# Kernel tuning notes

Measured on AMD Instinct MI355X. Metric: run time of the kernel, lower is better.

The kernel has to match this reference:

```python
import jax, jax.numpy as jnp
import numpy as np

B, C, H, W, A = 16, 4, 256, 256, 6
EPS = 1e-5


def _bn(z, s, b):
    # train-mode BatchNorm with batch size 1: reduce over (H, W) per channel, biased var
    m = z.mean((1, 2), keepdims=True)
    v = ((z - m) ** 2).mean((1, 2), keepdims=True)
    return (z - m) * jax.lax.rsqrt(v + EPS) * s[:, None, None] + b[:, None, None]


def _conv(z, w, pad, dil=1):
    # z: [C_in, H, W], w: [C_out, C_in, kh, kw]
    return jax.lax.conv_general_dilated(
        z[None], w, (1, 1), [(pad, pad), (pad, pad)],
        rhs_dilation=(dil, dil), dimension_numbers=("NCHW", "OIHW", "NCHW"))[0]


def _up2_axis(z, axis):
    # bilinear x2 with align_corners=True along one axis
    n = z.shape[axis]
    m = 2 * n
    pos = jnp.arange(m, dtype=jnp.float32) * ((n - 1) / (m - 1))
    i0 = jnp.floor(pos).astype(jnp.int32)
    i1 = jnp.minimum(i0 + 1, n - 1)
    f = pos - i0
    shape = [1] * z.ndim
    shape[axis] = m
    f = f.reshape(shape).astype(z.dtype)
    return jnp.take(z, i0, axis=axis) * (1 - f) + jnp.take(z, i1, axis=axis) * f


def _up2(z):
    return _up2_axis(_up2_axis(z, 1), 2)


def setup_inputs():
    key = jax.random.key(0)
    ks = jax.random.split(key, 16)
    inp = {}
    inp["x"] = jax.random.normal(ks[0], (B, C, H, W), jnp.float32)
    inp["action"] = jax.random.randint(ks[1], (B,), 0, A)
    # (out_features, init variance 2/(out_ch*k*k)) matching the torch init
    specs = [(16 * C * 25, 2.0 / (16 * 25)), (16 * 16 * 25, 2.0 / (16 * 25)),
             (32 * 16 * 25, 2.0 / (32 * 25)), (32 * 32 * 25, 2.0 / (32 * 25)),
             (64 * 32 * 25, 2.0 / (64 * 25)), (64 * 64 * 25, 2.0 / (64 * 25)),
             (4 * 64, 2.0 / 4.0)]
    for i, (od, var) in enumerate(specs):
        inp[f"w{i + 1}"] = jax.random.normal(ks[2 + i], (od, A), jnp.float32) * float(np.sqrt(var))
        inp[f"b{i + 1}"] = jnp.zeros((od,), jnp.float32)
    for i, ch in enumerate([C, 16, 16, 32, 32, 64, 64]):
        inp[f"bn{i}_s"] = jnp.ones((ch,), jnp.float32)
        inp[f"bn{i}_b"] = jnp.zeros((ch,), jnp.float32)
    return inp


def reference(x, action, w1, b1, w2, b2, w3, b3, w4, b4, w5, b5, w6, b6, w7, b7,
              bn0_s, bn0_b, bn1_s, bn1_b, bn2_s, bn2_b, bn3_s, bn3_b,
              bn4_s, bn4_b, bn5_s, bn5_b, bn6_s, bn6_b):
    onehot = jax.nn.one_hot(action, A, dtype=x.dtype)  # [B, A]

    def gen(w, b, shape):
        return (onehot @ w.T + b).reshape((x.shape[0],) + shape)

    y1 = gen(w1, b1, (16, C, 5, 5))
    y2 = gen(w2, b2, (16, 16, 5, 5))
    y3 = gen(w3, b3, (32, 16, 5, 5))
    y4 = gen(w4, b4, (32, 32, 5, 5))
    y5 = gen(w5, b5, (64, 32, 5, 5))
    y6 = gen(w6, b6, (64, 64, 5, 5))
    y7 = gen(w7, b7, (4, 64, 1, 1))

    def single(xi, k1, k2, k3, k4, k5, k6, k7):
        r = jax.nn.relu(_bn(_conv(_bn(xi, bn0_s, bn0_b), k1, 4, 2), bn1_s, bn1_b))
        r = _bn(_conv(r, k2, 2), bn2_s, bn2_b)
        c, h, w_ = r.shape  # avg_pool2d k=2 s=2
        r = r.reshape(c, h // 2, 2, w_ // 2, 2).mean((2, 4))
        r = jax.nn.relu(_bn(_conv(r, k3, 4, 2), bn3_s, bn3_b))
        r = _bn(_conv(r, k4, 2), bn4_s, bn4_b)
        r = jax.nn.relu(_bn(_conv(r, k5, 4, 2), bn5_s, bn5_b))
        r = _bn(_conv(r, k6, 2), bn6_s, bn6_b)
        r = _conv(r, k7, 0)  # 1x1 conv to `classes` channels
        return _up2(r)

    out = jax.vmap(single)(x, y1, y2, y3, y4, y5, y6, y7)
    return out + x
```

## Files before the change

### kernel.cpp

```cpp
#include <hip/hip_runtime.h>

#define NB 16
#define NA 6

typedef __attribute__((ext_vector_type(8))) short short8;
typedef __attribute__((ext_vector_type(4))) short short4_;
typedef __attribute__((ext_vector_type(4))) float f32x4;
typedef __attribute__((ext_vector_type(4))) unsigned uint4_;
typedef __attribute__((ext_vector_type(2))) unsigned uint2_;

__device__ __forceinline__ short tobf(float f) {
    unsigned u = __builtin_bit_cast(unsigned, f);
    u += 0x7FFF + ((u >> 16) & 1);
    return (short)(u >> 16);
}
__device__ __forceinline__ float frombf(short s) {
    unsigned u = ((unsigned)(unsigned short)s) << 16;
    return __builtin_bit_cast(float, u);
}
__device__ __forceinline__ unsigned cvtpk(float a, float b) {
    unsigned r;
    asm("v_cvt_pk_bf16_f32 %0, %1, %2" : "=v"(r) : "v"(a), "v"(b));
    return r;
}

template<int CIN, int COUT>
__device__ __forceinline__ void pack_one(const float* __restrict__ w, const float* __restrict__ bias,
                                         int a, int b, short* __restrict__ dst, int j) {
    constexpr int KTOT = 25 * CIN;
    constexpr int KPAD = (KTOT + 31) & ~31;
    if (j >= COUT * KPAD) return;
    int oc = j / KPAD, k = j - oc * KPAD;
    float v = 0.f;
    if (k < KTOT) {
        int pos = k / CIN, ci = k - pos * CIN;
        int ky = pos / 5, kx = pos - ky * 5;
        int od = ((oc * CIN + ci) * 5 + ky) * 5 + kx;
        v = w[(size_t)od * NA + a] + bias[od];
    }
    dst[((size_t)(b * (KPAD / 8) + (k >> 3)) * COUT + oc) * 8 + (k & 7)] = tobf(v);
}

__global__ void pack_all(const float* __restrict__ w2, const float* __restrict__ b2,
                         const float* __restrict__ w3, const float* __restrict__ b3,
                         const float* __restrict__ w4, const float* __restrict__ b4,
                         const float* __restrict__ w5, const float* __restrict__ b5,
                         const float* __restrict__ w6, const float* __restrict__ b6,
                         const float* __restrict__ w1, const float* __restrict__ b1,
                         const float* __restrict__ w7, const float* __restrict__ b7,
                         const int* __restrict__ action,
                         short* __restrict__ d2, short* __restrict__ d3, short* __restrict__ d4,
                         short* __restrict__ d5, short* __restrict__ d6,
                         float* __restrict__ g1, float* __restrict__ g7) {
    const int b = blockIdx.y;
    const int a = action[b];
    const int bx = blockIdx.x;
    const int t = threadIdx.x;
    if (bx < 26)       pack_one<16, 16>(w2, b2, a, b, d2, bx * 256 + t);
    else if (bx < 78)  pack_one<16, 32>(w3, b3, a, b, d3, (bx - 26) * 256 + t);
    else if (bx < 178) pack_one<32, 32>(w4, b4, a, b, d4, (bx - 78) * 256 + t);
    else if (bx < 378) pack_one<32, 64>(w5, b5, a, b, d5, (bx - 178) * 256 + t);
    else if (bx < 778) pack_one<64, 64>(w6, b6, a, b, d6, (bx - 378) * 256 + t);
    else if (bx < 785) { int i = (bx - 778) * 256 + t;
                         if (i < 1600) g1[(size_t)b * 1600 + i] = w1[(size_t)i * NA + a] + b1[i]; }
    else               { g7[(size_t)b * 256 + t] = w7[(size_t)t * NA + a] + b7[t]; }
}

__global__ void stats0(const float* __restrict__ x, float* __restrict__ part0) {
    const int bc = blockIdx.y;
    const int b = bc >> 2, c = bc & 3;
    const float* p = x + ((size_t)bc << 16);
    const int base = blockIdx.x * 4096;
    float sum = 0.f, sq = 0.f;
    for (int i = threadIdx.x * 4; i < 4096; i += 1024) {
        float4 v = *(const float4*)(p + base + i);
        sum += (v.x + v.y) + (v.z + v.w);
        sq  += (v.x * v.x + v.y * v.y) + (v.z * v.z + v.w * v.w);
    }
#pragma unroll
    for (int off = 32; off > 0; off >>= 1) {
        sum += __shfl_down(sum, off);
        sq  += __shfl_down(sq, off);
    }
    __shared__ float ssum[4], ssq[4];
    int wv = threadIdx.x >> 6;
    if ((threadIdx.x & 63) == 0) { ssum[wv] = sum; ssq[wv] = sq; }
    __syncthreads();
    if (threadIdx.x == 0) {
        float S = ssum[0] + ssum[1] + ssum[2] + ssum[3];
        float Q = ssq[0] + ssq[1] + ssq[2] + ssq[3];
        atomicAdd(&part0[((size_t)b * 2 + 0) * 4 + c], S);
        atomicAdd(&part0[((size_t)b * 2 + 1) * 4 + c], Q);
    }
}

__global__ void bn0_apply(const float* __restrict__ x, short* __restrict__ a0,
                          const float* __restrict__ part0,
                          const float* __restrict__ sc0, const float* __restrict__ bi0) {
    int t = blockIdx.x * 256 + threadIdx.x;
    int b = t >> 16, px = t & 65535;
    f32x4 g, e;
#pragma unroll
    for (int c = 0; c < 4; ++c) {
        float S0 = part0[((size_t)b * 2 + 0) * 4 + c];
        float Q0 = part0[((size_t)b * 2 + 1) * 4 + c];
        float m = S0 * (1.f / 65536.f);
        float var = Q0 * (1.f / 65536.f) - m * m;
        float gg = sc0[c] * rsqrtf(var + 1e-5f);
        g[c] = gg;
        e[c] = bi0[c] - m * gg;
    }
    f32x4 f;
#pragma unroll
    for (int c = 0; c < 4; ++c)
        f[c] = x[(((size_t)b * 4 + c) << 16) + px] * g[c] + e[c];
    uint2_ o = {cvtpk(f[0], f[1]), cvtpk(f[2], f[3])};
    *(uint2_*)&a0[((size_t)t) * 4] = o;
}

__global__ void __launch_bounds__(256) conv1k(const short* __restrict__ a0,
                                              const float* __restrict__ w1g,
                                              short* __restrict__ c1,
                                              float* __restrict__ partout) {
    __shared__ float wf[1600];
    __shared__ short4_ tile[16 * 72];
    const int b = blockIdx.z;
    const int y0 = blockIdx.y * 8;
    const int x0 = blockIdx.x * 64;
    const int tid = threadIdx.x;
    for (int t = tid; t < 1600; t += 256) {
        int pos = t >> 6, ci = (t >> 4) & 3, oc = t & 15;
        wf[t] = w1g[b * 1600 + (oc * 4 + ci) * 25 + pos];
    }
    const short* ab = a0 + ((size_t)b << 18);
    for (int idx = tid; idx < 16 * 72; idx += 256) {
        int r = idx / 72, cl = idx - r * 72;
        int gy = y0 - 4 + r, gx = x0 - 4 + cl;
        short4_ v = {0, 0, 0, 0};
        if ((unsigned)gy < 256u && (unsigned)gx < 256u)
            v = *(const short4_*)&ab[(((size_t)gy << 8) + gx) << 2];
        tile[idx] = v;
    }
    __syncthreads();
    const int wv = tid >> 6, xc = tid & 63;
    const int yr = wv * 2;
    f32x4 acc[2][4] = {};
#pragma unroll
    for (int ky = 0; ky < 5; ++ky) {
#pragma unroll
        for (int kx = 0; kx < 5; ++kx) {
            short4_ s0 = tile[(yr + 2 * ky) * 72 + xc + 2 * kx];
            short4_ s1 = tile[(yr + 1 + 2 * ky) * 72 + xc + 2 * kx];
            const int pos = ky * 5 + kx;
#pragma unroll
            for (int ci = 0; ci < 4; ++ci) {
                float f0 = frombf(s0[ci]);
                float f1 = frombf(s1[ci]);
                const float* wp = &wf[(pos * 4 + ci) * 16];
#pragma unroll
                for (int o = 0; o < 4; ++o) {
                    f32x4 w4 = *(const f32x4*)(wp + o * 4);
                    acc[0][o] += w4 * f0;
                    acc[1][o] += w4 * f1;
                }
            }
        }
    }
#pragma unroll
    for (int r = 0; r < 2; ++r) {
        size_t ob = ((size_t)b * 65536 + (size_t)(y0 + yr + r) * 256 + x0 + xc) * 16;
        uint4_ oA = {cvtpk(acc[r][0][0], acc[r][0][1]), cvtpk(acc[r][0][2], acc[r][0][3]),
                     cvtpk(acc[r][1][0], acc[r][1][1]), cvtpk(acc[r][1][2], acc[r][1][3])};
        uint4_ oB = {cvtpk(acc[r][2][0], acc[r][2][1]), cvtpk(acc[r][2][2], acc[r][2][3]),
                     cvtpk(acc[r][3][0], acc[r][3][1]), cvtpk(acc[r][3][2], acc[r][3][3])};
        *(uint4_*)&c1[ob] = oA;
        *(uint4_*)&c1[ob + 8] = oB;
    }
    float sv[16], qv[16];
#pragma unroll
    for (int o4 = 0; o4 < 4; ++o4)
#pragma unroll
        for (int j = 0; j < 4; ++j) {
            int o = o4 * 4 + j;
            float a0v = acc[0][o4][j], a1v = acc[1][o4][j];
            sv[o] = a0v + a1v;
            qv[o] = a0v * a0v + a1v * a1v;
        }
#pragma unroll
    for (int m = 1; m <= 32; m <<= 1)
#pragma unroll
        for (int o = 0; o < 16; ++o) {
            sv[o] += __shfl_xor(sv[o], m);
            qv[o] += __shfl_xor(qv[o], m);
        }
    __syncthreads();
    float* SPP = (float*)tile;
    if ((tid & 63) == 0) {
#pragma unroll
        for (int o = 0; o < 16; ++o) {
            SPP[wv * 32 + o] = sv[o];
            SPP[wv * 32 + 16 + o] = qv[o];
        }
    }
    __syncthreads();
    if (tid < 32) {
        int m = tid >> 4, c = tid & 15;
        float v = SPP[0 * 32 + m * 16 + c] + SPP[1 * 32 + m * 16 + c]
                + SPP[2 * 32 + m * 16 + c] + SPP[3 * 32 + m * 16 + c];
        atomicAdd(&partout[((size_t)b * 2 + m) * 16 + c], v);
    }
}

template<int C>
__device__ __forceinline__ void bn_fin8(const float* __restrict__ part,
                                        const float* __restrict__ sc,
                                        const float* __restrict__ bi,
                                        int b, int c0, float invN, f32x4* g, f32x4* e) {
#pragma unroll
    for (int h = 0; h < 2; ++h) {
        f32x4 Sv = *(const f32x4*)&part[((size_t)b * 2 + 0) * C + c0 + h * 4];
        f32x4 Qv = *(const f32x4*)&part[((size_t)b * 2 + 1) * C + c0 + h * 4];
        f32x4 scv = *(const f32x4*)&sc[c0 + h * 4];
        f32x4 biv = *(const f32x4*)&bi[c0 + h * 4];
#pragma unroll
        for (int j = 0; j < 4; ++j) {
            float m = Sv[j] * invN;
            float var = Qv[j] * invN - m * m;
            float gg = scv[j] * rsqrtf(var + 1e-5f);
            g[h][j] = gg;
            e[h][j] = biv[j] - m * gg;
        }
    }
}

__global__ void bnpool2(const short* __restrict__ in, short* __restrict__ out,
                        const float* __restrict__ part, const float* __restrict__ sc,
                        const float* __restrict__ bi) {
    const int b = blockIdx.y;
    const int c8 = threadIdx.x & 1;
    const int c0 = c8 * 8;
    f32x4 g[2], e[2];
    bn_fin8<16>(part, sc, bi, b, c0, 1.f / 65536.f, g, e);
    const size_t bin = (size_t)b * 65536 * 16;
    const size_t bout = (size_t)b * 16384 * 16;
    int total = 16384 * 2;
    int stride = gridDim.x * 256;
    for (int i = blockIdx.x * 256 + threadIdx.x; i < total; i += stride) {
        int opx = i >> 1;
        int ho = opx >> 7, wo = opx & 127;
        size_t p0 = bin + ((size_t)(ho * 2) * 256 + wo * 2) * 16 + c0;
        short8 v00 = *(const short8*)&in[p0];
        short8 v01 = *(const short8*)&in[p0 + 16];
        short8 v10 = *(const short8*)&in[p0 + 4096];
        short8 v11 = *(const short8*)&in[p0 + 4112];
        float f[8];
#pragma unroll
        for (int h = 0; h < 2; ++h)
#pragma unroll
            for (int j = 0; j < 4; ++j) {
                int k = h * 4 + j;
                float fv = (frombf(v00[k]) + frombf(v01[k]) + frombf(v10[k]) + frombf(v11[k])) * 0.25f;
                f[k] = fv * g[h][j] + e[h][j];
            }
        uint4_ vo = {cvtpk(f[0], f[1]), cvtpk(f[2], f[3]), cvtpk(f[4], f[5]), cvtpk(f[6], f[7])};
        *(uint4_*)&out[bout + (size_t)i * 8] = vo;
    }
}

template<int CIN, int COUT, int DIL, int WH, int PXB, int ROWS, int OCG, int WAVES, int APPLY>
__global__ void __launch_bounds__(WAVES * 64) convmf7(const short* __restrict__ in,
                                                      const short* __restrict__ wpack,
                                                      short* __restrict__ outp,
                                                      float* __restrict__ partout,
                                                      const float* __restrict__ partin,
                                                      const float* __restrict__ psc,
                                                      const float* __restrict__ pbi,
                                                      float invN) {
    constexpr int PAD   = 2 * DIL;
    constexpr int XT    = PXB + 4 * DIL + 1;
    constexpr int LROWS = (DIL == 1) ? (ROWS + 4) : 5 * ROWS;
    constexpr int RSTR  = (DIL == 1) ? XT : 5 * XT;
    constexpr int KTOT  = 25 * CIN;
    constexpr int KPAD  = (KTOT + 31) & ~31;
    constexpr int NSTEP = KPAD / 32;
    constexpr int CINB  = CIN / 8;
    constexpr int S     = (CIN == 64) ? 0 : (CIN == 32) ? 1 : 2;
    constexpr int NTHR  = WAVES * 64;
    constexpr int PXG   = WAVES / OCG;
    constexpr int OT    = COUT / 16 / OCG;
    constexpr int PT    = ROWS * PXB / (16 * PXG);
    constexpr int LPXB  = (PXB == 32) ? 5 : (PXB == 64) ? 6 : 7;
    constexpr int LOGC  = (COUT == 64) ? 6 : (COUT == 32) ? 5 : 4;
    constexpr int TBYTES = LROWS * XT * CIN * 2;
    static_assert(PXG * 2 * COUT * 4 <= TBYTES, "SP alias fits in T");
    static_assert(NSTEP >= 2, "pipeline depth");
    static_assert(PT * 16 * PXG == ROWS * PXB, "px cover");

    __shared__ __align__(16) char smem[TBYTES + 2 * CIN * 4];
    short* T  = (short*)smem;
    float* GA = (float*)(smem + TBYTES);
    float* BE = GA + CIN;
    float* SP = (float*)smem;

    const int b   = blockIdx.z;
    const int y0  = blockIdx.y * ROWS;
    const int x0  = blockIdx.x * PXB;
    const int tid = threadIdx.x;

    if (APPLY) {
        if (tid < CIN) {
            float S0 = partin[((size_t)b * 2 + 0) * CIN + tid];
            float Q0 = partin[((size_t)b * 2 + 1) * CIN + tid];
            float m = S0 * invN;
            float var = Q0 * invN - m * m;
            float g = psc[tid] * rsqrtf(var + 1e-5f);
            GA[tid] = g;
            BE[tid] = pbi[tid] - m * g;
        }
        __syncthreads();
    }

    const short* inb = in + (size_t)b * WH * WH * CIN;
    for (int idx = tid; idx < LROWS * XT * CINB; idx += NTHR) {
        int dyi = idx / (XT * CINB);
        int rem = idx - dyi * (XT * CINB);
        int xl = rem / CINB, cic = rem - xl * CINB;
        int gy;
        if (DIL == 1) gy = y0 + dyi - 2;
        else          gy = y0 + dyi / 5 + 2 * (dyi % 5) - 4;
        int gx = x0 - PAD + xl;
        short8 v = {};
        if ((unsigned)gy < (unsigned)WH && (unsigned)gx < (unsigned)WH) {
            v = *(const short8*)&inb[((size_t)gy * WH + gx) * CIN + cic * 8];
            if (APPLY) {
                float f[8];
#pragma unroll
                for (int j = 0; j < 8; ++j) f[j] = frombf(v[j]);
                f32x4 g0 = *(const f32x4*)&GA[cic * 8];
                f32x4 g1 = *(const f32x4*)&GA[cic * 8 + 4];
                f32x4 e0 = *(const f32x4*)&BE[cic * 8];
                f32x4 e1 = *(const f32x4*)&BE[cic * 8 + 4];
#pragma unroll
                for (int j = 0; j < 4; ++j) {
                    f[j]     = f[j]     * g0[j] + e0[j];
                    f[4 + j] = f[4 + j] * g1[j] + e1[j];
                    if (APPLY == 2) { f[j] = fmaxf(f[j], 0.f); f[4 + j] = fmaxf(f[4 + j], 0.f); }
                }
                uint4_ uv = {cvtpk(f[0], f[1]), cvtpk(f[2], f[3]),
                             cvtpk(f[4], f[5]), cvtpk(f[6], f[7])};
                v = __builtin_bit_cast(short8, uv);
            }
        }
        int r = dyi * XT + xl;
        int cs = (cic ^ ((r >> S) & (CINB - 1))) << 3;
        *(short8*)&T[r * CIN + cs] = v;
    }
    __syncthreads();

    const int w = tid >> 6, lane = tid & 63;
    const int l15 = lane & 15, loct = lane >> 4;
    const int ocg = w & (OCG - 1);
    const int pxg = w / OCG;
    const int ocbase = ocg * OT * 16;
    const int pxbase = pxg * PT * 16;
    const int hsel = loct >> 1;

    int bpt[PT];
#pragma unroll
    for (int pt = 0; pt < PT; ++pt) {
        int ppx = pxbase + pt * 16;
        bpt[pt] = (ppx >> LPXB) * RSTR + (ppx & (PXB - 1)) + l15;
    }

    const short* wl = wpack + (size_t)b * KPAD * COUT + ((size_t)loct * COUT + ocbase + l15) * 8;

    auto lA = [&](int s, short8* dst) {
        const short* ws = wl + (size_t)s * (4 * COUT * 8);
#pragma unroll
        for (int ot = 0; ot < OT; ++ot) dst[ot] = *(const short8*)&ws[ot * 128];
    };
    auto lB = [&](int s, short8* dst) {
        int Cs, cic;
        if constexpr (CIN == 64) {
            const int pos = s >> 1;
            Cs = (pos / 5) * XT + (pos % 5) * DIL;
            cic = (s & 1) * 4 + loct;
        } else if constexpr (CIN == 32) {
            Cs = (s / 5) * XT + (s % 5) * DIL;
            cic = loct;
        } else {
            const int p0 = (2 * s > 24) ? 24 : 2 * s;
            const int p1 = (2 * s + 1 > 24) ? 24 : 2 * s + 1;
            const int C0 = (p0 / 5) * XT + (p0 % 5) * DIL;
            const int C1 = (p1 / 5) * XT + (p1 % 5) * DIL;
            Cs = hsel ? C1 : C0;
            cic = loct & 1;
        }
#pragma unroll
        for (int pt = 0; pt < PT; ++pt) {
            int r = bpt[pt] + Cs;
            int chunk = cic ^ ((r >> S) & (CINB - 1));
            dst[pt] = *(const short8*)&T[r * CIN + (chunk << 3)];
        }
    };

    f32x4 acc[OT][PT] = {};
    short8 Acur[OT], Anx[OT], Bcur[PT];
    lA(0, Acur);
    lA(1, Anx);
    lB(0, Bcur);

    __builtin_amdgcn_s_setprio(1);
#pragma unroll
    for (int s = 0; s < NSTEP; ++s) {
        short8 An2[OT] = {}, Bn[PT] = {};
        if (s + 2 < NSTEP) lA(s + 2, An2);
        if (s + 1 < NSTEP) lB(s + 1, Bn);
#pragma unroll
        for (int ot = 0; ot < OT; ++ot)
#pragma unroll
            for (int pt = 0; pt < PT; ++pt)
                acc[ot][pt] = __builtin_amdgcn_mfma_f32_16x16x32_bf16(Acur[ot], Bcur[pt], acc[ot][pt], 0, 0, 0);
#pragma unroll
        for (int ot = 0; ot < OT; ++ot) { Acur[ot] = Anx[ot]; Anx[ot] = An2[ot]; }
#pragma unroll
        for (int pt = 0; pt < PT; ++pt) Bcur[pt] = Bn[pt];
    }
    __builtin_amdgcn_s_setprio(0);

#pragma unroll
    for (int ot = 0; ot < OT; ++ot)
#pragma unroll
        for (int pt = 0; pt < PT; ++pt) {
            int ppx = pxbase + pt * 16;
            int gpx = (y0 + (ppx >> LPXB)) * WH + x0 + (ppx & (PXB - 1)) + l15;
            int oc = ocbase + ot * 16 + (loct << 2);
            uint2_ st = {cvtpk(acc[ot][pt][0], acc[ot][pt][1]),
                         cvtpk(acc[ot][pt][2], acc[ot][pt][3])};
            *(uint2_*)&outp[((size_t)b * WH * WH + gpx) * COUT + oc] = st;
        }

    __syncthreads();

    float sv[OT][4], qv[OT][4];
#pragma unroll
    for (int ot = 0; ot < OT; ++ot)
#pragma unroll
        for (int j = 0; j < 4; ++j) {
            float sa = 0.f, qa = 0.f;
#pragma unroll
            for (int pt = 0; pt < PT; ++pt) { float v = acc[ot][pt][j]; sa += v; qa += v * v; }
#pragma unroll
            for (int m = 1; m <= 8; m <<= 1) { sa += __shfl_xor(sa, m); qa += __shfl_xor(qa, m); }
            sv[ot][j] = sa; qv[ot][j] = qa;
        }
    if (l15 == 0) {
#pragma unroll
        for (int ot = 0; ot < OT; ++ot)
#pragma unroll
            for (int j = 0; j < 4; ++j) {
                int c = ocbase + ot * 16 + (loct << 2) + j;
                SP[(pxg * 2 + 0) * COUT + c] = sv[ot][j];
                SP[(pxg * 2 + 1) * COUT + c] = qv[ot][j];
            }
    }
    __syncthreads();
    if (tid < 2 * COUT) {
        int m = tid >> LOGC, c = tid & (COUT - 1);
        float v = 0.f;
#pragma unroll
        for (int g = 0; g < PXG; ++g) v += SP[(g * 2 + m) * COUT + c];
        atomicAdd(&partout[((size_t)b * 2 + m) * COUT + c], v);
    }
}

__global__ void conv7k(const short* __restrict__ c6, const float* __restrict__ w7g,
                       const float* __restrict__ part, const float* __restrict__ sc,
                       const float* __restrict__ bi, float* __restrict__ c7) {
    __shared__ float wsm[256];
    __shared__ float GA[64], BE[64];
    const int b = blockIdx.y;
    const int t = threadIdx.x;
    wsm[t] = w7g[b * 256 + t];
    if (t < 64) {
        float S0 = part[((size_t)b * 2 + 0) * 64 + t];
        float Q0 = part[((size_t)b * 2 + 1) * 64 + t];
        float m = S0 * (1.f / 16384.f);
        float var = Q0 * (1.f / 16384.f) - m * m;
        float g = sc[t] * rsqrtf(var + 1e-5f);
        GA[t] = g;
        BE[t] = bi[t] - m * g;
    }
    __syncthreads();
    const int px = blockIdx.x * 64 + (t >> 2);
    const int q4 = t & 3;
    size_t base = ((size_t)b * 16384 + px) * 64 + q4 * 16;
    short8 s0 = *(const short8*)&c6[base];
    short8 s1 = *(const short8*)&c6[base + 8];
    f32x4 a = {0.f, 0.f, 0.f, 0.f};
#pragma unroll
    for (int ci = 0; ci < 8; ++ci) {
        float f0 = frombf(s0[ci]) * GA[q4 * 16 + ci] + BE[q4 * 16 + ci];
        float f1 = frombf(s1[ci]) * GA[q4 * 16 + 8 + ci] + BE[q4 * 16 + 8 + ci];
#pragma unroll
        for (int o = 0; o < 4; ++o) {
            a[o] = fmaf(f0, wsm[o * 64 + q4 * 16 + ci], a[o]);
            a[o] = fmaf(f1, wsm[o * 64 + q4 * 16 + 8 + ci], a[o]);
        }
    }
#pragma unroll
    for (int o = 0; o < 4; ++o) {
        a[o] += __shfl_xor(a[o], 1);
        a[o] += __shfl_xor(a[o], 2);
    }
    if (q4 == 0) *(f32x4*)&c7[((size_t)b * 16384 + px) * 4] = a;
}

__global__ void up2_add(const float* __restrict__ h, const float* __restrict__ xin,
                        float* __restrict__ outp, int total) {
    int stride = gridDim.x * blockDim.x;
    const float sc = 127.f / 255.f;
    for (int i = blockIdx.x * blockDim.x + threadIdx.x; i < total; i += stride) {
        int xo = i & 255, yo = (i >> 8) & 255, c = (i >> 16) & 3, b = i >> 18;
        float px = xo * sc, py = yo * sc;
        int x0 = (int)px, y0 = (int)py;
        float fx = px - x0, fy = py - y0;
        int x1 = min(x0 + 1, 127), y1 = min(y0 + 1, 127);
        const float* hb = h + ((size_t)b << 16);
        float v00 = hb[((y0 << 7) + x0) * 4 + c], v01 = hb[((y0 << 7) + x1) * 4 + c];
        float v10 = hb[((y1 << 7) + x0) * 4 + c], v11 = hb[((y1 << 7) + x1) * 4 + c];
        float vt = v00 + (v01 - v00) * fx;
        float vb = v10 + (v11 - v10) * fx;
        outp[i] = vt + (vb - vt) * fy + xin[i];
    }
}

extern "C" void kernel_launch(void* const* d_in, const int* in_sizes, int n_in,
                              void* d_out, int out_size, void* d_ws, size_t ws_size,
                              hipStream_t stream) {
    const float* x = (const float*)d_in[0];
    const int* action = (const int*)d_in[1];
    const float *W[7], *Bi[7], *bns[7], *bnb[7];
    for (int i = 0; i < 7; ++i) { W[i]   = (const float*)d_in[2 + 2 * i];
                                  Bi[i]  = (const float*)d_in[3 + 2 * i]; }
    for (int i = 0; i < 7; ++i) { bns[i] = (const float*)d_in[16 + 2 * i];
                                  bnb[i] = (const float*)d_in[17 + 2 * i]; }
    float* out = (float*)d_out;

    char* p = (char*)d_ws;
    auto carve = [&](size_t bytes) { char* r = p; p += (bytes + 255) & ~(size_t)255; return r; };
    float* w1g  = (float*)carve(1600 * NB * 4);
    float* w7g  = (float*)carve(256 * NB * 4);
    float* partAll = (float*)carve((size_t)NB * 2 * 228 * 4);
    float* p0 = partAll;
    float* p1 = p0 + NB * 2 * 4;
    float* p2 = p1 + NB * 2 * 16;
    float* p3 = p2 + NB * 2 * 16;
    float* p4 = p3 + NB * 2 * 32;
    float* p5 = p4 + NB * 2 * 32;
    float* p6 = p5 + NB * 2 * 64;
    short* wp2  = (short*)carve((size_t)416 * 16 * NB * 2);
    short* wp3  = (short*)carve((size_t)416 * 32 * NB * 2);
    short* wp4  = (short*)carve((size_t)800 * 32 * NB * 2);
    short* wp5  = (short*)carve((size_t)800 * 64 * NB * 2);
    short* wp6  = (short*)carve((size_t)1600 * 64 * NB * 2);
    short* CB_A = (short*)carve((size_t)NB * 65536 * 16 * 2);
    short* CB_B = (short*)carve((size_t)NB * 65536 * 16 * 2);
    short* A0   = (short*)carve((size_t)NB * 65536 * 4 * 2);
    float* C7   = (float*)carve((size_t)NB * 16384 * 4 * 4);

    hipMemsetAsync(partAll, 0, (size_t)NB * 2 * 228 * 4, stream);

    pack_all<<<dim3(786, NB), 256, 0, stream>>>(
        W[1], Bi[1], W[2], Bi[2], W[3], Bi[3], W[4], Bi[4], W[5], Bi[5],
        W[0], Bi[0], W[6], Bi[6], action, wp2, wp3, wp4, wp5, wp6, w1g, w7g);

    stats0<<<dim3(16, 64), 256, 0, stream>>>(x, p0);
    bn0_apply<<<4096, 256, 0, stream>>>(x, A0, p0, bns[0], bnb[0]);

    conv1k<<<dim3(4, 32, NB), 256, 0, stream>>>(A0, w1g, CB_A, p1);

    convmf7<16, 16, 1, 256, 32, 16, 1, 8, 2><<<dim3(8, 16, NB), 512, 0, stream>>>(
        CB_A, wp2, CB_B, p2, p1, bns[1], bnb[1], 1.f / 65536.f);

    bnpool2<<<dim3(64, NB), 256, 0, stream>>>(CB_B, A0, p2, bns[2], bnb[2]);

    convmf7<16, 32, 2, 128, 128, 2, 1, 8, 0><<<dim3(1, 64, NB), 512, 0, stream>>>(
        A0, wp3, CB_A, p3, p2, bns[2], bnb[2], 1.f);

    convmf7<32, 32, 1, 128, 64, 8, 1, 8, 2><<<dim3(2, 16, NB), 512, 0, stream>>>(
        CB_A, wp4, CB_B, p4, p3, bns[3], bnb[3], 1.f / 16384.f);

    convmf7<32, 64, 2, 128, 128, 1, 2, 4, 1><<<dim3(1, 128, NB), 256, 0, stream>>>(
        CB_B, wp5, CB_A, p5, p4, bns[4], bnb[4], 1.f / 16384.f);

    convmf7<64, 64, 1, 128, 32, 8, 2, 8, 2><<<dim3(4, 16, NB), 512, 0, stream>>>(
        CB_A, wp6, CB_B, p6, p5, bns[5], bnb[5], 1.f / 16384.f);

    conv7k<<<dim3(256, NB), 256, 0, stream>>>(CB_B, w7g, p6, bns[6], bnb[6], C7);
    up2_add<<<4096, 256, 0, stream>>>(C7, x, out, 4194304);
}
```

Before: 313.6 us.

## Fuse BN0 apply into first conv and run conv1 on MFMA path

Removes the separate bn0_apply pass and the scalar FP32 conv1k kernel. The first dilated 5x5 conv now goes through the templated MFMA conv kernel with a new input mode that reads fp32 x directly, applies BN0 in the tile load, and pads the 4 channels to 8. Conv1 weights are packed into a bf16 MFMA layout with zero-padded channels. This cuts a full write and read of the intermediate activation and moves conv1 onto matrix cores, at the cost of wasted MFMA work on the padded channels and strided fp32 loads.

```diff
diff --git a/kernel.cpp b/kernel.cpp
--- a/kernel.cpp
+++ b/kernel.cpp
@@ -41,6 +41,22 @@
     dst[((size_t)(b * (KPAD / 8) + (k >> 3)) * COUT + oc) * 8 + (k & 7)] = tobf(v);
 }
 
+__device__ __forceinline__ void pack_one8(const float* __restrict__ w, const float* __restrict__ bias,
+                                          int a, int b, short* __restrict__ dst, int j) {
+    if (j >= 16 * 224) return;
+    int oc = j / 224, k = j - oc * 224;
+    float v = 0.f;
+    if (k < 200) {
+        int pos = k >> 3, ci = k & 7;
+        if (ci < 4) {
+            int ky = pos / 5, kx = pos - ky * 5;
+            int od = ((oc * 4 + ci) * 5 + ky) * 5 + kx;
+            v = w[(size_t)od * NA + a] + bias[od];
+        }
+    }
+    dst[((size_t)(b * 28 + (k >> 3)) * 16 + oc) * 8 + (k & 7)] = tobf(v);
+}
+
 __global__ void pack_all(const float* __restrict__ w2, const float* __restrict__ b2,
                          const float* __restrict__ w3, const float* __restrict__ b3,
                          const float* __restrict__ w4, const float* __restrict__ b4,
@@ -51,7 +67,7 @@
                          const int* __restrict__ action,
                          short* __restrict__ d2, short* __restrict__ d3, short* __restrict__ d4,
                          short* __restrict__ d5, short* __restrict__ d6,
-                         float* __restrict__ g1, float* __restrict__ g7) {
+                         short* __restrict__ d1, float* __restrict__ g7) {
     const int b = blockIdx.y;
     const int a = action[b];
     const int bx = blockIdx.x;
@@ -61,8 +77,7 @@
     else if (bx < 178) pack_one<32, 32>(w4, b4, a, b, d4, (bx - 78) * 256 + t);
     else if (bx < 378) pack_one<32, 64>(w5, b5, a, b, d5, (bx - 178) * 256 + t);
     else if (bx < 778) pack_one<64, 64>(w6, b6, a, b, d6, (bx - 378) * 256 + t);
-    else if (bx < 785) { int i = (bx - 778) * 256 + t;
-                         if (i < 1600) g1[(size_t)b * 1600 + i] = w1[(size_t)i * NA + a] + b1[i]; }
+    else if (bx < 792) pack_one8(w1, b1, a, b, d1, (bx - 778) * 256 + t);
     else               { g7[(size_t)b * 256 + t] = w7[(size_t)t * NA + a] + b7[t]; }
 }
 
@@ -91,123 +106,6 @@
         float Q = ssq[0] + ssq[1] + ssq[2] + ssq[3];
         atomicAdd(&part0[((size_t)b * 2 + 0) * 4 + c], S);
         atomicAdd(&part0[((size_t)b * 2 + 1) * 4 + c], Q);
-    }
-}
-
-__global__ void bn0_apply(const float* __restrict__ x, short* __restrict__ a0,
-                          const float* __restrict__ part0,
-                          const float* __restrict__ sc0, const float* __restrict__ bi0) {
-    int t = blockIdx.x * 256 + threadIdx.x;
-    int b = t >> 16, px = t & 65535;
-    f32x4 g, e;
-#pragma unroll
-    for (int c = 0; c < 4; ++c) {
-        float S0 = part0[((size_t)b * 2 + 0) * 4 + c];
-        float Q0 = part0[((size_t)b * 2 + 1) * 4 + c];
-        float m = S0 * (1.f / 65536.f);
-        float var = Q0 * (1.f / 65536.f) - m * m;
-        float gg = sc0[c] * rsqrtf(var + 1e-5f);
-        g[c] = gg;
-        e[c] = bi0[c] - m * gg;
-    }
-    f32x4 f;
-#pragma unroll
-    for (int c = 0; c < 4; ++c)
-        f[c] = x[(((size_t)b * 4 + c) << 16) + px] * g[c] + e[c];
-    uint2_ o = {cvtpk(f[0], f[1]), cvtpk(f[2], f[3])};
-    *(uint2_*)&a0[((size_t)t) * 4] = o;
-}
-
-__global__ void __launch_bounds__(256) conv1k(const short* __restrict__ a0,
-                                              const float* __restrict__ w1g,
-                                              short* __restrict__ c1,
-                                              float* __restrict__ partout) {
-    __shared__ float wf[1600];
-    __shared__ short4_ tile[16 * 72];
-    const int b = blockIdx.z;
-    const int y0 = blockIdx.y * 8;
-    const int x0 = blockIdx.x * 64;
-    const int tid = threadIdx.x;
-    for (int t = tid; t < 1600; t += 256) {
-        int pos = t >> 6, ci = (t >> 4) & 3, oc = t & 15;
-        wf[t] = w1g[b * 1600 + (oc * 4 + ci) * 25 + pos];
-    }
-    const short* ab = a0 + ((size_t)b << 18);
-    for (int idx = tid; idx < 16 * 72; idx += 256) {
-        int r = idx / 72, cl = idx - r * 72;
-        int gy = y0 - 4 + r, gx = x0 - 4 + cl;
-        short4_ v = {0, 0, 0, 0};
-        if ((unsigned)gy < 256u && (unsigned)gx < 256u)
-            v = *(const short4_*)&ab[(((size_t)gy << 8) + gx) << 2];
-        tile[idx] = v;
-    }
-    __syncthreads();
-    const int wv = tid >> 6, xc = tid & 63;
-    const int yr = wv * 2;
-    f32x4 acc[2][4] = {};
-#pragma unroll
-    for (int ky = 0; ky < 5; ++ky) {
-#pragma unroll
-        for (int kx = 0; kx < 5; ++kx) {
-            short4_ s0 = tile[(yr + 2 * ky) * 72 + xc + 2 * kx];
-            short4_ s1 = tile[(yr + 1 + 2 * ky) * 72 + xc + 2 * kx];
-            const int pos = ky * 5 + kx;
-#pragma unroll
-            for (int ci = 0; ci < 4; ++ci) {
-                float f0 = frombf(s0[ci]);
-                float f1 = frombf(s1[ci]);
-                const float* wp = &wf[(pos * 4 + ci) * 16];
-#pragma unroll
-                for (int o = 0; o < 4; ++o) {
-                    f32x4 w4 = *(const f32x4*)(wp + o * 4);
-                    acc[0][o] += w4 * f0;
-                    acc[1][o] += w4 * f1;
-                }
-            }
-        }
-    }
-#pragma unroll
-    for (int r = 0; r < 2; ++r) {
-        size_t ob = ((size_t)b * 65536 + (size_t)(y0 + yr + r) * 256 + x0 + xc) * 16;
-        uint4_ oA = {cvtpk(acc[r][0][0], acc[r][0][1]), cvtpk(acc[r][0][2], acc[r][0][3]),
-                     cvtpk(acc[r][1][0], acc[r][1][1]), cvtpk(acc[r][1][2], acc[r][1][3])};
-        uint4_ oB = {cvtpk(acc[r][2][0], acc[r][2][1]), cvtpk(acc[r][2][2], acc[r][2][3]),
-                     cvtpk(acc[r][3][0], acc[r][3][1]), cvtpk(acc[r][3][2], acc[r][3][3])};
-        *(uint4_*)&c1[ob] = oA;
-        *(uint4_*)&c1[ob + 8] = oB;
-    }
-    float sv[16], qv[16];
-#pragma unroll
-    for (int o4 = 0; o4 < 4; ++o4)
-#pragma unroll
-        for (int j = 0; j < 4; ++j) {
-            int o = o4 * 4 + j;
-            float a0v = acc[0][o4][j], a1v = acc[1][o4][j];
-            sv[o] = a0v + a1v;
-            qv[o] = a0v * a0v + a1v * a1v;
-        }
-#pragma unroll
-    for (int m = 1; m <= 32; m <<= 1)
-#pragma unroll
-        for (int o = 0; o < 16; ++o) {
-            sv[o] += __shfl_xor(sv[o], m);
-            qv[o] += __shfl_xor(qv[o], m);
-        }
-    __syncthreads();
-    float* SPP = (float*)tile;
-    if ((tid & 63) == 0) {
-#pragma unroll
-        for (int o = 0; o < 16; ++o) {
-            SPP[wv * 32 + o] = sv[o];
-            SPP[wv * 32 + 16 + o] = qv[o];
-        }
-    }
-    __syncthreads();
-    if (tid < 32) {
-        int m = tid >> 4, c = tid & 15;
-        float v = SPP[0 * 32 + m * 16 + c] + SPP[1 * 32 + m * 16 + c]
-                + SPP[2 * 32 + m * 16 + c] + SPP[3 * 32 + m * 16 + c];
-        atomicAdd(&partout[((size_t)b * 2 + m) * 16 + c], v);
     }
 }
 
@@ -267,8 +165,8 @@
     }
 }
 
-template<int CIN, int COUT, int DIL, int WH, int PXB, int ROWS, int OCG, int WAVES, int APPLY>
-__global__ void __launch_bounds__(WAVES * 64) convmf7(const short* __restrict__ in,
+template<int CIN, int COUT, int DIL, int WH, int PXB, int ROWS, int OCG, int WAVES, int APPLY, int INMODE = 0>
+__global__ void __launch_bounds__(WAVES * 64) convmf8(const short* __restrict__ in,
                                                       const short* __restrict__ wpack,
                                                       short* __restrict__ outp,
                                                       float* __restrict__ partout,
@@ -291,15 +189,16 @@
     constexpr int PT    = ROWS * PXB / (16 * PXG);
     constexpr int LPXB  = (PXB == 32) ? 5 : (PXB == 64) ? 6 : 7;
     constexpr int LOGC  = (COUT == 64) ? 6 : (COUT == 32) ? 5 : 4;
+    constexpr int CREAL = (INMODE == 1) ? 4 : CIN;
     constexpr int TBYTES = LROWS * XT * CIN * 2;
     static_assert(PXG * 2 * COUT * 4 <= TBYTES, "SP alias fits in T");
     static_assert(NSTEP >= 2, "pipeline depth");
     static_assert(PT * 16 * PXG == ROWS * PXB, "px cover");
 
-    __shared__ __align__(16) char smem[TBYTES + 2 * CIN * 4];
+    __shared__ __align__(16) char smem[TBYTES + 2 * 64 * 4];
     short* T  = (short*)smem;
     float* GA = (float*)(smem + TBYTES);
-    float* BE = GA + CIN;
+    float* BE = GA + 64;
     float* SP = (float*)smem;
 
     const int b   = blockIdx.z;
@@ -308,9 +207,9 @@
     const int tid = threadIdx.x;
 
     if (APPLY) {
-        if (tid < CIN) {
-            float S0 = partin[((size_t)b * 2 + 0) * CIN + tid];
-            float Q0 = partin[((size_t)b * 2 + 1) * CIN + tid];
+        if (tid < CREAL) {
+            float S0 = partin[((size_t)b * 2 + 0) * CREAL + tid];
+            float Q0 = partin[((size_t)b * 2 + 1) * CREAL + tid];
             float m = S0 * invN;
             float var = Q0 * invN - m * m;
             float g = psc[tid] * rsqrtf(var + 1e-5f);
@@ -320,40 +219,62 @@
         __syncthreads();
     }
 
-    const short* inb = in + (size_t)b * WH * WH * CIN;
-    for (int idx = tid; idx < LROWS * XT * CINB; idx += NTHR) {
-        int dyi = idx / (XT * CINB);
-        int rem = idx - dyi * (XT * CINB);
-        int xl = rem / CINB, cic = rem - xl * CINB;
-        int gy;
-        if (DIL == 1) gy = y0 + dyi - 2;
-        else          gy = y0 + dyi / 5 + 2 * (dyi % 5) - 4;
-        int gx = x0 - PAD + xl;
-        short8 v = {};
-        if ((unsigned)gy < (unsigned)WH && (unsigned)gx < (unsigned)WH) {
-            v = *(const short8*)&inb[((size_t)gy * WH + gx) * CIN + cic * 8];
-            if (APPLY) {
-                float f[8];
-#pragma unroll
-                for (int j = 0; j < 8; ++j) f[j] = frombf(v[j]);
-                f32x4 g0 = *(const f32x4*)&GA[cic * 8];
-                f32x4 g1 = *(const f32x4*)&GA[cic * 8 + 4];
-                f32x4 e0 = *(const f32x4*)&BE[cic * 8];
-                f32x4 e1 = *(const f32x4*)&BE[cic * 8 + 4];
-#pragma unroll
-                for (int j = 0; j < 4; ++j) {
-                    f[j]     = f[j]     * g0[j] + e0[j];
-                    f[4 + j] = f[4 + j] * g1[j] + e1[j];
-                    if (APPLY == 2) { f[j] = fmaxf(f[j], 0.f); f[4 + j] = fmaxf(f[4 + j], 0.f); }
-                }
-                uint4_ uv = {cvtpk(f[0], f[1]), cvtpk(f[2], f[3]),
-                             cvtpk(f[4], f[5]), cvtpk(f[6], f[7])};
+    if constexpr (INMODE == 1) {
+        const float* xf = (const float*)in + ((size_t)b << 18);
+        float g0 = GA[0], g1 = GA[1], g2 = GA[2], g3 = GA[3];
+        float e0 = BE[0], e1 = BE[1], e2 = BE[2], e3 = BE[3];
+        for (int idx = tid; idx < LROWS * XT; idx += NTHR) {
+            int dyi = idx / XT, xl = idx - dyi * XT;
+            int gy = (DIL == 1) ? (y0 + dyi - 2) : (y0 + dyi / 5 + 2 * (dyi % 5) - 4);
+            int gx = x0 - PAD + xl;
+            short8 v = {};
+            if ((unsigned)gy < (unsigned)WH && (unsigned)gx < (unsigned)WH) {
+                int o = (gy << 8) + gx;
+                float f0 = xf[o] * g0 + e0;
+                float f1 = xf[o + 65536] * g1 + e1;
+                float f2 = xf[o + 131072] * g2 + e2;
+                float f3 = xf[o + 196608] * g3 + e3;
+                uint4_ uv = {cvtpk(f0, f1), cvtpk(f2, f3), 0u, 0u};
                 v = __builtin_bit_cast(short8, uv);
             }
-        }
-        int r = dyi * XT + xl;
-        int cs = (cic ^ ((r >> S) & (CINB - 1))) << 3;
-        *(short8*)&T[r * CIN + cs] = v;
+            *(short8*)&T[idx * CIN] = v;
+        }
+    } else {
+        const short* inb = in + (size_t)b * WH * WH * CIN;
+        for (int idx = tid; idx < LROWS * XT * CINB; idx += NTHR) {
+            int dyi = idx / (XT * CINB);
+            int rem = idx - dyi * (XT * CINB);
+            int xl = rem / CINB, cic = rem - xl * CINB;
+            int gy;
+            if (DIL == 1) gy = y0 + dyi - 2;
+            else          gy = y0 + dyi / 5 + 2 * (dyi % 5) - 4;
+            int gx = x0 - PAD + xl;
+            short8 v = {};
+            if ((unsigned)gy < (unsigned)WH && (unsigned)gx < (unsigned)WH) {
+                v = *(const short8*)&inb[((size_t)gy * WH + gx) * CIN + cic * 8];
+                if (APPLY) {
+                    float f[8];
+#pragma unroll
+                    for (int j = 0; j < 8; ++j) f[j] = frombf(v[j]);
+                    f32x4 g0 = *(const f32x4*)&GA[cic * 8];
+                    f32x4 g1 = *(const f32x4*)&GA[cic * 8 + 4];
+                    f32x4 e0 = *(const f32x4*)&BE[cic * 8];
+                    f32x4 e1 = *(const f32x4*)&BE[cic * 8 + 4];
+#pragma unroll
+                    for (int j = 0; j < 4; ++j) {
+                        f[j]     = f[j]     * g0[j] + e0[j];
+                        f[4 + j] = f[4 + j] * g1[j] + e1[j];
+                        if (APPLY == 2) { f[j] = fmaxf(f[j], 0.f); f[4 + j] = fmaxf(f[4 + j], 0.f); }
+                    }
+                    uint4_ uv = {cvtpk(f[0], f[1]), cvtpk(f[2], f[3]),
+                                 cvtpk(f[4], f[5]), cvtpk(f[6], f[7])};
+                    v = __builtin_bit_cast(short8, uv);
+                }
+            }
+            int r = dyi * XT + xl;
+            int cs = (cic ^ ((r >> S) & (CINB - 1))) << 3;
+            *(short8*)&T[r * CIN + cs] = v;
+        }
     }
     __syncthreads();
 
@@ -364,6 +285,7 @@
     const int ocbase = ocg * OT * 16;
     const int pxbase = pxg * PT * 16;
     const int hsel = loct >> 1;
+    (void)hsel;
 
     int bpt[PT];
 #pragma unroll
@@ -388,6 +310,11 @@
         } else if constexpr (CIN == 32) {
             Cs = (s / 5) * XT + (s % 5) * DIL;
             cic = loct;
+        } else if constexpr (CIN == 8) {
+            int pos = s * 4 + loct;
+            if (pos > 24) pos = 24;
+            Cs = (pos / 5) * XT + (pos % 5) * DIL;
+            cic = 0;
         } else {
             const int p0 = (2 * s > 24) ? 24 : 2 * s;
             const int p1 = (2 * s + 1 > 24) ? 24 : 2 * s + 1;
@@ -549,7 +476,6 @@
 
     char* p = (char*)d_ws;
     auto carve = [&](size_t bytes) { char* r = p; p += (bytes + 255) & ~(size_t)255; return r; };
-    float* w1g  = (float*)carve(1600 * NB * 4);
     float* w7g  = (float*)carve(256 * NB * 4);
     float* partAll = (float*)carve((size_t)NB * 2 * 228 * 4);
     float* p0 = partAll;
@@ -559,6 +485,7 @@
     float* p4 = p3 + NB * 2 * 32;
     float* p5 = p4 + NB * 2 * 32;
     float* p6 = p5 + NB * 2 * 64;
+    short* wp1  = (short*)carve((size_t)224 * 16 * NB * 2);
     short* wp2  = (short*)carve((size_t)416 * 16 * NB * 2);
     short* wp3  = (short*)carve((size_t)416 * 32 * NB * 2);
     short* wp4  = (short*)carve((size_t)800 * 32 * NB * 2);
@@ -571,30 +498,30 @@
 
     hipMemsetAsync(partAll, 0, (size_t)NB * 2 * 228 * 4, stream);
 
-    pack_all<<<dim3(786, NB), 256, 0, stream>>>(
+    pack_all<<<dim3(793, NB), 256, 0, stream>>>(
         W[1], Bi[1], W[2], Bi[2], W[3], Bi[3], W[4], Bi[4], W[5], Bi[5],
-        W[0], Bi[0], W[6], Bi[6], action, wp2, wp3, wp4, wp5, wp6, w1g, w7g);
+        W[0], Bi[0], W[6], Bi[6], action, wp2, wp3, wp4, wp5, wp6, wp1, w7g);
 
     stats0<<<dim3(16, 64), 256, 0, stream>>>(x, p0);
-    bn0_apply<<<4096, 256, 0, stream>>>(x, A0, p0, bns[0], bnb[0]);
-
-    conv1k<<<dim3(4, 32, NB), 256, 0, stream>>>(A0, w1g, CB_A, p1);
-
-    convmf7<16, 16, 1, 256, 32, 16, 1, 8, 2><<<dim3(8, 16, NB), 512, 0, stream>>>(
+
+    convmf8<8, 16, 2, 256, 128, 2, 1, 8, 1, 1><<<dim3(2, 128, NB), 512, 0, stream>>>(
+        (const short*)x, wp1, CB_A, p1, p0, bns[0], bnb[0], 1.f / 65536.f);
+
+    convmf8<16, 16, 1, 256, 32, 16, 1, 8, 2><<<dim3(8, 16, NB), 512, 0, stream>>>(
         CB_A, wp2, CB_B, p2, p1, bns[1], bnb[1], 1.f / 65536.f);
 
     bnpool2<<<dim3(64, NB), 256, 0, stream>>>(CB_B, A0, p2, bns[2], bnb[2]);
 
-    convmf7<16, 32, 2, 128, 128, 2, 1, 8, 0><<<dim3(1, 64, NB), 512, 0, stream>>>(
+    convmf8<16, 32, 2, 128, 128, 2, 1, 8, 0><<<dim3(1, 64, NB), 512, 0, stream>>>(
         A0, wp3, CB_A, p3, p2, bns[2], bnb[2], 1.f);
 
-    convmf7<32, 32, 1, 128, 64, 8, 1, 8, 2><<<dim3(2, 16, NB), 512, 0, stream>>>(
+    convmf8<32, 32, 1, 128, 64, 8, 1, 8, 2><<<dim3(2, 16, NB), 512, 0, stream>>>(
         CB_A, wp4, CB_B, p4, p3, bns[3], bnb[3], 1.f / 16384.f);
 
-    convmf7<32, 64, 2, 128, 128, 1, 2, 4, 1><<<dim3(1, 128, NB), 256, 0, stream>>>(
+    convmf8<32, 64, 2, 128, 128, 1, 2, 4, 1><<<dim3(1, 128, NB), 256, 0, stream>>>(
         CB_B, wp5, CB_A, p5, p4, bns[4], bnb[4], 1.f / 16384.f);
 
-    convmf7<64, 64, 1, 128, 32, 8, 2, 8, 2><<<dim3(4, 16, NB), 512, 0, stream>>>(
+    convmf8<64, 64, 1, 128, 32, 8, 2, 8, 2><<<dim3(4, 16, NB), 512, 0, stream>>>(
         CB_A, wp6, CB_B, p6, p5, bns[5], bnb[5], 1.f / 16384.f);
 
     conv7k<<<dim3(256, NB), 256, 0, stream>>>(CB_B, w7g, p6, bns[6], bnb[6], C7);
```

Measured after the change: 278.4 us (median of 2 runs). 11.2% less time.
